# Performance work log

Measured on AMD Instinct MI355X. Metric: run time of the kernel, lower is better.

## Reference

```python
import jax, jax.numpy as jnp
import numpy as np

N = 4096
NODE_DIM = 256
HIDDEN = 64
N_CLASSES = 16
N_HEADS = 4
NEG_SLOPE = 0.01  # F.leaky_relu default


def _xavier(key, shape):
    fan_out, fan_in = shape[0], shape[1]
    limit = float(np.sqrt(6.0 / (fan_in + fan_out)))
    return jax.random.uniform(key, shape, jnp.float32, -limit, limit)


def setup_inputs() -> dict:
    key = jax.random.key(0)
    ks = jax.random.split(key, 8)
    x = jax.random.normal(ks[0], (N, NODE_DIM), jnp.float32)
    adj_mat = jax.random.randint(ks[1], (N, N), 0, 2, jnp.int32)
    # head-stacked layer-1 params
    W1 = _xavier(ks[2], (N_HEADS * HIDDEN, NODE_DIM)).reshape(N_HEADS, HIDDEN, NODE_DIM)
    a1_1 = _xavier(ks[3], (N_HEADS * HIDDEN, 1)).reshape(N_HEADS, HIDDEN)
    a2_1 = _xavier(ks[4], (N_HEADS * HIDDEN, 1)).reshape(N_HEADS, HIDDEN)
    # layer-2 params
    W2 = _xavier(ks[5], (N_CLASSES, N_HEADS * HIDDEN))
    a1_2 = _xavier(ks[6], (N_CLASSES, 1))[:, 0]
    a2_2 = _xavier(ks[7], (N_CLASSES, 1))[:, 0]
    return {"x": x, "adj_mat": adj_mat, "W1": W1, "a1_1": a1_1, "a2_1": a2_1,
            "W2": W2, "a1_2": a1_2, "a2_2": a2_2}


def _attention_layer(x, adj_f, W, a1, a2):
    # x: [N, in_dim], W: [out_dim, in_dim], a1/a2: [out_dim]
    h = x @ W.T                               # [N, d]
    f1 = h @ a1                               # [N]
    f2 = h @ a2                               # [N]
    e = jax.nn.leaky_relu(f1[:, None] + f2[None, :], NEG_SLOPE)  # [N, N]
    e = e * adj_f
    e = jnp.where(e == 0, -jnp.inf, e)        # faithful to torch.where(e==0, -inf, e)
    alpha = jax.nn.softmax(e, axis=1)         # [N, N]
    return alpha @ h                          # [N, d]


def reference(x, adj_mat, W1, a1_1, a2_1, W2, a1_2, a2_2):
    adj_f = adj_mat.astype(x.dtype)
    # layer 1: vmap over heads, concat along feature dim
    heads = jax.vmap(_attention_layer, in_axes=(None, None, 0, 0, 0))(
        x, adj_f, W1, a1_1, a2_1)              # [H, N, hidden]
    h = jnp.transpose(heads, (1, 0, 2)).reshape(N, N_HEADS * HIDDEN)
    h = jax.nn.elu(h)
    # dropout p=0.0 -> identity
    logits = _attention_layer(h, adj_f, W2, a1_2, a2_2)  # [N, n_classes]
    return logits
```

## Files before the change

kernel.cpp:

```cpp
#include <hip/hip_runtime.h>
#include <cstdint>

typedef __bf16 bf16x8 __attribute__((ext_vector_type(8)));
typedef float  f32x4  __attribute__((ext_vector_type(4)));

#define LOG2E 1.4426950408889634f

__device__ __forceinline__ void split8(const float* v, bf16x8& hi, bf16x8& lo) {
    union { bf16x8 v; __bf16 e[8]; } h, l;
    #pragma unroll
    for (int j = 0; j < 8; j++) {
        __bf16 hb = (__bf16)v[j];
        float  r  = v[j] - (float)hb;
        h.e[j] = hb; l.e[j] = (__bf16)r;
    }
    hi = h.v; lo = l.v;
}
__device__ __forceinline__ bf16x8 cvt8(const float* v) {
    union { bf16x8 v; __bf16 e[8]; } u;
    #pragma unroll
    for (int j = 0; j < 8; j++) u.e[j] = (__bf16)v[j];
    return u.v;
}
__device__ __forceinline__ void splitstore(unsigned short* ph, unsigned short* pl, float v) {
    __bf16 hb = (__bf16)v;
    float  r  = v - (float)hb;
    __bf16 lb = (__bf16)r;
    unsigned short hu, lu;
    __builtin_memcpy(&hu, &hb, 2); __builtin_memcpy(&lu, &lb, 2);
    *ph = hu; *pl = lu;
}
__device__ __forceinline__ unsigned short f2bfh(float v) {
    __bf16 hb = (__bf16)v; unsigned short hu;
    __builtin_memcpy(&hu, &hb, 2); return hu;
}

__global__ __launch_bounds__(256)
void kzero(float4* __restrict__ p) {
    p[blockIdx.x * 256 + threadIdx.x] = float4{0.f, 0.f, 0.f, 0.f};
}

__global__ __launch_bounds__(256)
void kpre(const int* __restrict__ adj, unsigned long long* __restrict__ bm64,
          const float* __restrict__ w1, const float* __restrict__ w2,
          unsigned short* __restrict__ w1h, unsigned short* __restrict__ w1l,
          unsigned short* __restrict__ w2h, unsigned short* __restrict__ w2l) {
    int bx = blockIdx.x, tid = threadIdx.x;
    if (bx < 8192) {
        int row = bx >> 1, jbase = (bx & 1) * 2048;
        int wave = tid >> 6, lane = tid & 63;
        const int* base = adj + (size_t)row * 4096 + jbase + wave * 512;
        unsigned long long* bmw = bm64 + row * 64 + (jbase >> 6) + wave * 8;
        #pragma unroll
        for (int it = 0; it < 8; it++) {
            int v = base[it * 64 + lane];
            unsigned long long mask = __ballot(v != 0);
            if (lane == 0) bmw[it] = mask;
        }
        return;
    }
    int e = ((bx - 8192) * 256 + tid) * 4;
    const float* src; unsigned short *dh, *dl;
    if (e < 65536) { src = w1 + e; dh = w1h + e; dl = w1l + e; }
    else { int e2 = e - 65536; src = w2 + e2; dh = w2h + e2; dl = w2l + e2; }
    #pragma unroll
    for (int j = 0; j < 4; j++) splitstore(dh + j, dl + j, src[j]);
}

__global__ __launch_bounds__(256)
void k1_gemm(const float* __restrict__ x,
             const unsigned short* __restrict__ w1h,
             const unsigned short* __restrict__ w1l,
             const float* __restrict__ a11, const float* __restrict__ a21,
             unsigned short* __restrict__ h1t_hi, float* __restrict__ fvals) {
    int tid = threadIdx.x, wave = tid >> 6, lane = tid & 63;
    int q = lane >> 4, m = lane & 15;
    int i0 = blockIdx.x * 16;
    int c0 = wave * 64;
    f32x4 acc[4] = {};
    #pragma unroll
    for (int k0 = 0; k0 < 256; k0 += 32) {
        bf16x8 ah, al;
        split8(x + (i0 + m) * 256 + k0 + q * 8, ah, al);
        #pragma unroll
        for (int ct = 0; ct < 4; ct++) {
            bf16x8 bh = *(const bf16x8*)(w1h + (c0 + ct * 16 + m) * 256 + k0 + q * 8);
            bf16x8 bl = *(const bf16x8*)(w1l + (c0 + ct * 16 + m) * 256 + k0 + q * 8);
            acc[ct] = __builtin_amdgcn_mfma_f32_16x16x32_bf16(ah, bh, acc[ct], 0, 0, 0);
            acc[ct] = __builtin_amdgcn_mfma_f32_16x16x32_bf16(al, bh, acc[ct], 0, 0, 0);
            acc[ct] = __builtin_amdgcn_mfma_f32_16x16x32_bf16(ah, bl, acc[ct], 0, 0, 0);
        }
    }
    float a1v[4], a2v[4];
    #pragma unroll
    for (int ct = 0; ct < 4; ct++) {
        a1v[ct] = a11[wave * 64 + ct * 16 + m];
        a2v[ct] = a21[wave * 64 + ct * 16 + m];
    }
    #pragma unroll
    for (int r = 0; r < 4; r++) {
        int i = i0 + q * 4 + r;
        float s1 = 0.f, s2 = 0.f;
        #pragma unroll
        for (int ct = 0; ct < 4; ct++) {
            int c = c0 + ct * 16 + m;
            h1t_hi[c * 4096 + i] = f2bfh(acc[ct][r]);
            s1 += acc[ct][r] * a1v[ct];
            s2 += acc[ct][r] * a2v[ct];
        }
        #pragma unroll
        for (int off = 1; off < 16; off <<= 1) {
            s1 += __shfl_xor(s1, off);
            s2 += __shfl_xor(s2, off);
        }
        if (m == 0) {
            fvals[wave * 4096 + i] = s1 * LOG2E;
            fvals[16384 + wave * 4096 + i] = s2 * LOG2E;
        }
    }
}

template<int NCT, int JLEN, bool ATOM>
__global__ __launch_bounds__(256)
void attn_kernel(const unsigned char* __restrict__ bmb,
                 const float* __restrict__ f1_all,
                 const float* __restrict__ f2_all,
                 const unsigned short* __restrict__ BTh_all,
                 float* __restrict__ pacc,
                 float* __restrict__ zacc,
                 int pstride) {
    constexpr int S    = JLEN / 32;
    constexpr int ST   = (S % 8 == 0) ? S + 4 : S;
    constexpr int PR   = S / 4;
    constexpr int R    = 64;
    constexpr int NU4  = R * PR;
    constexpr int CR   = NCT * 16;
    constexpr int TSTR = 40;
    constexpr int NIT  = JLEN / 32;
    int tid = threadIdx.x, wave = tid >> 6, lane = tid & 63;
    int q = lane >> 4, m = lane & 15;
    int head = blockIdx.y;
    int i0 = blockIdx.x * R;
    int jstart = blockIdx.z * JLEN;

    if (!ATOM) {
        pacc += (size_t)blockIdx.z * (size_t)(4096 * pstride);
        zacc += (size_t)blockIdx.z * (size_t)((NCT == 4 ? 4 : 1) * 4096);
    }

    __shared__ unsigned int ldsbm[R * ST];
    __shared__ unsigned short ldsbt[2][CR * TSTR];
    __shared__ float ldsf2[JLEN];

    const unsigned short* BTh = BTh_all + (size_t)head * CR * 4096;
    const float* f1 = f1_all + head * 4096;
    const float* f2 = f2_all + head * 4096;

    for (int c = tid; c < NU4; c += 256) {
        int row = c / PR, part = c % PR;
        uint4 v = *(const uint4*)(bmb + (size_t)(i0 + row) * 512 + (jstart >> 3) + part * 16);
        *(uint4*)&ldsbm[row * ST + part * 4] = v;
    }
    for (int c = tid; c < JLEN / 4; c += 256)
        *(float4*)&ldsf2[c * 4] = *(const float4*)(f2 + jstart + c * 4);

    int sc = tid >> 2, sp = tid & 3;
    bool stager = tid < CR * 4;
    const unsigned short* sbase = BTh + (size_t)sc * 4096 + jstart + sp * 8;
    unsigned short* swr = &ldsbt[0][0] + sc * TSTR + sp * 8;

    uint4 vA, vB;
    if (stager) {
        uint4 v0 = *(const uint4*)(sbase);
        *(uint4*)(swr) = v0;
        if (NIT > 1) vB = *(const uint4*)(sbase + 32);
    }

    int col0 = head * CR;
    int r0 = wave * 16;
    float f1s0 = f1[i0 + r0 + m];

    f32x4 acc0[NCT] = {};
    float z0 = 0.f;

    constexpr int BUFO = CR * TSTR;

    auto body = [&](int it, uint4& vpre, uint4& vwr) {
        __syncthreads();
        int jl = it * 32;
        if (stager && it + 2 < NIT)
            vpre = *(const uint4*)(sbase + jl + 64);
        unsigned int md0 = ldsbm[(r0 + m) * ST + it];
        const float4* f2p = (const float4*)&ldsf2[jl + q * 8];
        float4 fa = f2p[0], fb = f2p[1];
        float fv[8] = {fa.x, fa.y, fa.z, fa.w, fb.x, fb.y, fb.z, fb.w};
        float pv0[8];
        #pragma unroll
        for (int jj = 0; jj < 8; jj++) {
            int bit = q * 8 + jj;
            float s0 = f1s0 + fv[jj];
            float e0 = fmaxf(s0, 0.01f * s0);
            bool v0 = ((md0 >> bit) & 1u) && (s0 != 0.0f);
            float p0 = v0 ? __builtin_amdgcn_exp2f(e0) : 0.0f;
            z0 += p0; pv0[jj] = p0;
        }
        bf16x8 ah0 = cvt8(pv0);
        int cur = it & 1;
        const unsigned short* rb = &ldsbt[0][0] + cur * BUFO;
        #pragma unroll
        for (int ct = 0; ct < NCT; ct++) {
            bf16x8 bh = *(const bf16x8*)(rb + (ct * 16 + m) * TSTR + q * 8);
            acc0[ct] = __builtin_amdgcn_mfma_f32_16x16x32_bf16(ah0, bh, acc0[ct], 0, 0, 0);
        }
        if (stager && it + 1 < NIT)
            *(uint4*)(swr + (1 - cur) * BUFO) = vwr;
    };

    for (int itp = 0; itp < NIT; itp += 2) {
        body(itp,     vA, vB);
        body(itp + 1, vB, vA);
    }

    z0 += __shfl_xor(z0, 16); z0 += __shfl_xor(z0, 32);
    if (lane < 16) {
        if (ATOM) {
            atomicAdd(&zacc[head * 4096 + i0 + r0 + lane], z0);
        } else {
            zacc[head * 4096 + i0 + r0 + lane] = z0;
        }
    }
    #pragma unroll
    for (int ct = 0; ct < NCT; ct++)
        #pragma unroll
        for (int r = 0; r < 4; r++) {
            int col = col0 + ct * 16 + m;
            int rowA = i0 + r0 + q * 4 + r;
            if (ATOM) {
                atomicAdd(&pacc[rowA * pstride + col], acc0[ct][r]);
            } else {
                pacc[rowA * pstride + col] = acc0[ct][r];
            }
        }
}

__global__ __launch_bounds__(256)
void fin1c(const float* __restrict__ pp, const float* __restrict__ zp, int nj,
           unsigned short* __restrict__ hh, unsigned short* __restrict__ hl) {
    int row = blockIdx.x, col = threadIdx.x;
    float s = 0.f;
    for (int jc = 0; jc < nj; jc++) s += pp[(size_t)jc * (4096 * 256) + row * 256 + col];
    int head = col >> 6;
    float zz = 0.f;
    for (int jc = 0; jc < nj; jc++) zz += zp[jc * (4 * 4096) + head * 4096 + row];
    float v = s / zz;
    v = (v > 0.f) ? v : (__expf(v) - 1.0f);
    splitstore(&hh[row * 256 + col], &hl[row * 256 + col], v);
}

__global__ __launch_bounds__(256)
void k3_layer2(const unsigned short* __restrict__ helu_hi,
               const unsigned short* __restrict__ helu_lo,
               const unsigned short* __restrict__ w2h,
               const unsigned short* __restrict__ w2l,
               const float* __restrict__ a12,
               const float* __restrict__ a22,
               unsigned short* __restrict__ h2t_hi,
               float* __restrict__ fq) {
    int tid = threadIdx.x, wave = tid >> 6, lane = tid & 63;
    int q = lane >> 4, m = lane & 15;
    int i0 = (blockIdx.x * 4 + wave) * 16;
    f32x4 acc = {};
    #pragma unroll
    for (int k0 = 0; k0 < 256; k0 += 32) {
        bf16x8 ah = *(const bf16x8*)(helu_hi + (i0 + m) * 256 + k0 + q * 8);
        bf16x8 al = *(const bf16x8*)(helu_lo + (i0 + m) * 256 + k0 + q * 8);
        bf16x8 bh = *(const bf16x8*)(w2h + m * 256 + k0 + q * 8);
        bf16x8 bl = *(const bf16x8*)(w2l + m * 256 + k0 + q * 8);
        acc = __builtin_amdgcn_mfma_f32_16x16x32_bf16(ah, bh, acc, 0, 0, 0);
        acc = __builtin_amdgcn_mfma_f32_16x16x32_bf16(al, bh, acc, 0, 0, 0);
        acc = __builtin_amdgcn_mfma_f32_16x16x32_bf16(ah, bl, acc, 0, 0, 0);
    }
    float a1v = a12[m], a2v = a22[m];
    #pragma unroll
    for (int r = 0; r < 4; r++) {
        float v = acc[r];
        int i = i0 + q * 4 + r;
        h2t_hi[m * 4096 + i] = f2bfh(v);
        float s1 = v * a1v, s2 = v * a2v;
        #pragma unroll
        for (int off = 1; off < 16; off <<= 1) {
            s1 += __shfl_xor(s1, off);
            s2 += __shfl_xor(s2, off);
        }
        if (m == 0) { fq[i] = s1 * LOG2E; fq[4096 + i] = s2 * LOG2E; }
    }
}

__global__ __launch_bounds__(256)
void fin2(const float* __restrict__ pp, const float* __restrict__ zp, int nj,
          float* __restrict__ out) {
    int idx = blockIdx.x * 256 + threadIdx.x;
    float s = 0.f;
    for (int jc = 0; jc < nj; jc++) s += pp[jc * 65536 + idx];
    float zz = 0.f;
    for (int jc = 0; jc < nj; jc++) zz += zp[jc * 4096 + (idx >> 4)];
    out[idx] = s / zz;
}

extern "C" void kernel_launch(void* const* d_in, const int* in_sizes, int n_in,
                              void* d_out, int out_size, void* d_ws, size_t ws_size,
                              hipStream_t stream) {
    const float* x   = (const float*)d_in[0];
    const int*   adj = (const int*)d_in[1];
    const float* w1  = (const float*)d_in[2];
    const float* a11 = (const float*)d_in[3];
    const float* a21 = (const float*)d_in[4];
    const float* w2  = (const float*)d_in[5];
    const float* a12 = (const float*)d_in[6];
    const float* a22 = (const float*)d_in[7];
    float* out = (float*)d_out;

    uint8_t* w = (uint8_t*)d_ws;
    unsigned long long* bm  = (unsigned long long*)(w);
    unsigned short* h1t_hi  = (unsigned short*)(w + (2u << 20));
    unsigned short* h2t_hi  = (unsigned short*)(w + (4u << 20));
    float*          fvals   = (float*)(w + (4u << 20) + (128u << 10));
    float*          fq      = (float*)(w + (4u << 20) + (256u << 10));
    unsigned short* w1h     = (unsigned short*)(w + (4u << 20) + (288u << 10));
    unsigned short* w1l     = (unsigned short*)(w + (4u << 20) + (416u << 10));
    unsigned short* w2h     = (unsigned short*)(w + (4u << 20) + (544u << 10));
    unsigned short* w2l     = (unsigned short*)(w + (4u << 20) + (552u << 10));
    unsigned short* helu_hi = (unsigned short*)(w + (4u << 20) + (560u << 10));
    unsigned short* helu_lo = (unsigned short*)(w + (4u << 20) + (2608u << 10));

    bool big = ws_size >= ((size_t)48 << 20);
    float* p1 = (float*)(w + (9u << 20));
    float *z1, *p2, *z2;
    if (big) {
        z1 = p1 + (size_t)4 * 4096 * 256;
        p2 = z1 + 4 * 4 * 4096;
        z2 = p2 + (size_t)16 * 4096 * 16;
    } else {
        z1 = p1 + 4096 * 256;
        p2 = z1 + 4 * 4096;
        z2 = p2 + 4096 * 16;
    }

    if (!big) kzero<<<1108, 256, 0, stream>>>((float4*)p1);
    kpre<<<8260, 256, 0, stream>>>(adj, bm, w1, w2, w1h, w1l, w2h, w2l);
    k1_gemm<<<256, 256, 0, stream>>>(x, w1h, w1l, a11, a21, h1t_hi, fvals);
    if (big)
        attn_kernel<4, 1024, false><<<dim3(64, 4, 4), 256, 0, stream>>>(
            (const unsigned char*)bm, fvals, fvals + 16384, h1t_hi, p1, z1, 256);
    else
        attn_kernel<4, 1024, true><<<dim3(64, 4, 4), 256, 0, stream>>>(
            (const unsigned char*)bm, fvals, fvals + 16384, h1t_hi, p1, z1, 256);
    fin1c<<<4096, 256, 0, stream>>>(p1, z1, big ? 4 : 1, helu_hi, helu_lo);
    k3_layer2<<<64, 256, 0, stream>>>(helu_hi, helu_lo, w2h, w2l, a12, a22,
                                      h2t_hi, fq);
    if (big)
        attn_kernel<1, 256, false><<<dim3(64, 1, 16), 256, 0, stream>>>(
            (const unsigned char*)bm, fq, fq + 4096, h2t_hi, p2, z2, 16);
    else
        attn_kernel<1, 256, true><<<dim3(64, 1, 16), 256, 0, stream>>>(
            (const unsigned char*)bm, fq, fq + 4096, h2t_hi, p2, z2, 16);
    fin2<<<256, 256, 0, stream>>>(p2, z2, big ? 16 : 1, out);
}
```

Measured before the change: 190.9 us.

## Fuse layer-1 GEMM into adjacency prep and widen attention K-step to 64

Merges the weight-splitting preprocessing and the layer-1 GEMM into the adjacency bitmask kernel. The GEMM blocks now split W1 to hi/lo bf16 inline, and layer 2 splits W2 inline too, which removes a launch and the workspace round-trip for the split weights. The attention kernel now stages 64-column tiles per iteration with two 32-column MFMA sub-steps, and replaces __syncthreads with explicit lgkmcnt waits plus raw s_barrier, halving the number of barriers. The trade-off is redundant W1 conversion work in every GEMM block and larger LDS tiles, and the hand-placed waits risk subtle synchronization errors.

```diff
diff --git a/kernel.cpp b/kernel.cpp
--- a/kernel.cpp
+++ b/kernel.cpp
@@ -5,6 +5,8 @@
 typedef float  f32x4  __attribute__((ext_vector_type(4)));
 
 #define LOG2E 1.4426950408889634f
+#define LGKM0 do { asm volatile("s_waitcnt lgkmcnt(0)" ::: "memory"); \
+                   __builtin_amdgcn_sched_barrier(0); } while (0)
 
 __device__ __forceinline__ void split8(const float* v, bf16x8& hi, bf16x8& lo) {
     union { bf16x8 v; __bf16 e[8]; } h, l;
@@ -41,82 +43,69 @@
 }
 
 __global__ __launch_bounds__(256)
-void kpre(const int* __restrict__ adj, unsigned long long* __restrict__ bm64,
-          const float* __restrict__ w1, const float* __restrict__ w2,
-          unsigned short* __restrict__ w1h, unsigned short* __restrict__ w1l,
-          unsigned short* __restrict__ w2h, unsigned short* __restrict__ w2l) {
+void kpre2(const int* __restrict__ adj, unsigned long long* __restrict__ bm64,
+           const float* __restrict__ x, const float* __restrict__ w1,
+           const float* __restrict__ a11, const float* __restrict__ a21,
+           unsigned short* __restrict__ h1t_hi, float* __restrict__ fvals) {
     int bx = blockIdx.x, tid = threadIdx.x;
-    if (bx < 8192) {
-        int row = bx >> 1, jbase = (bx & 1) * 2048;
+    if (bx < 256) {
         int wave = tid >> 6, lane = tid & 63;
-        const int* base = adj + (size_t)row * 4096 + jbase + wave * 512;
-        unsigned long long* bmw = bm64 + row * 64 + (jbase >> 6) + wave * 8;
-        #pragma unroll
-        for (int it = 0; it < 8; it++) {
-            int v = base[it * 64 + lane];
-            unsigned long long mask = __ballot(v != 0);
-            if (lane == 0) bmw[it] = mask;
+        int q = lane >> 4, m = lane & 15;
+        int i0 = bx * 16;
+        int c0 = wave * 64;
+        f32x4 acc[4] = {};
+        #pragma unroll
+        for (int k0 = 0; k0 < 256; k0 += 32) {
+            bf16x8 ah, al;
+            split8(x + (i0 + m) * 256 + k0 + q * 8, ah, al);
+            #pragma unroll
+            for (int ct = 0; ct < 4; ct++) {
+                bf16x8 bh, bl;
+                split8(w1 + (c0 + ct * 16 + m) * 256 + k0 + q * 8, bh, bl);
+                acc[ct] = __builtin_amdgcn_mfma_f32_16x16x32_bf16(ah, bh, acc[ct], 0, 0, 0);
+                acc[ct] = __builtin_amdgcn_mfma_f32_16x16x32_bf16(al, bh, acc[ct], 0, 0, 0);
+                acc[ct] = __builtin_amdgcn_mfma_f32_16x16x32_bf16(ah, bl, acc[ct], 0, 0, 0);
+            }
+        }
+        float a1v[4], a2v[4];
+        #pragma unroll
+        for (int ct = 0; ct < 4; ct++) {
+            a1v[ct] = a11[wave * 64 + ct * 16 + m];
+            a2v[ct] = a21[wave * 64 + ct * 16 + m];
+        }
+        #pragma unroll
+        for (int r = 0; r < 4; r++) {
+            int i = i0 + q * 4 + r;
+            float s1 = 0.f, s2 = 0.f;
+            #pragma unroll
+            for (int ct = 0; ct < 4; ct++) {
+                int c = c0 + ct * 16 + m;
+                h1t_hi[c * 4096 + i] = f2bfh(acc[ct][r]);
+                s1 += acc[ct][r] * a1v[ct];
+                s2 += acc[ct][r] * a2v[ct];
+            }
+            #pragma unroll
+            for (int off = 1; off < 16; off <<= 1) {
+                s1 += __shfl_xor(s1, off);
+                s2 += __shfl_xor(s2, off);
+            }
+            if (m == 0) {
+                fvals[wave * 4096 + i] = s1 * LOG2E;
+                fvals[16384 + wave * 4096 + i] = s2 * LOG2E;
+            }
         }
         return;
     }
-    int e = ((bx - 8192) * 256 + tid) * 4;
-    const float* src; unsigned short *dh, *dl;
-    if (e < 65536) { src = w1 + e; dh = w1h + e; dl = w1l + e; }
-    else { int e2 = e - 65536; src = w2 + e2; dh = w2h + e2; dl = w2l + e2; }
-    #pragma unroll
-    for (int j = 0; j < 4; j++) splitstore(dh + j, dl + j, src[j]);
-}
-
-__global__ __launch_bounds__(256)
-void k1_gemm(const float* __restrict__ x,
-             const unsigned short* __restrict__ w1h,
-             const unsigned short* __restrict__ w1l,
-             const float* __restrict__ a11, const float* __restrict__ a21,
-             unsigned short* __restrict__ h1t_hi, float* __restrict__ fvals) {
-    int tid = threadIdx.x, wave = tid >> 6, lane = tid & 63;
-    int q = lane >> 4, m = lane & 15;
-    int i0 = blockIdx.x * 16;
-    int c0 = wave * 64;
-    f32x4 acc[4] = {};
-    #pragma unroll
-    for (int k0 = 0; k0 < 256; k0 += 32) {
-        bf16x8 ah, al;
-        split8(x + (i0 + m) * 256 + k0 + q * 8, ah, al);
-        #pragma unroll
-        for (int ct = 0; ct < 4; ct++) {
-            bf16x8 bh = *(const bf16x8*)(w1h + (c0 + ct * 16 + m) * 256 + k0 + q * 8);
-            bf16x8 bl = *(const bf16x8*)(w1l + (c0 + ct * 16 + m) * 256 + k0 + q * 8);
-            acc[ct] = __builtin_amdgcn_mfma_f32_16x16x32_bf16(ah, bh, acc[ct], 0, 0, 0);
-            acc[ct] = __builtin_amdgcn_mfma_f32_16x16x32_bf16(al, bh, acc[ct], 0, 0, 0);
-            acc[ct] = __builtin_amdgcn_mfma_f32_16x16x32_bf16(ah, bl, acc[ct], 0, 0, 0);
-        }
-    }
-    float a1v[4], a2v[4];
-    #pragma unroll
-    for (int ct = 0; ct < 4; ct++) {
-        a1v[ct] = a11[wave * 64 + ct * 16 + m];
-        a2v[ct] = a21[wave * 64 + ct * 16 + m];
-    }
-    #pragma unroll
-    for (int r = 0; r < 4; r++) {
-        int i = i0 + q * 4 + r;
-        float s1 = 0.f, s2 = 0.f;
-        #pragma unroll
-        for (int ct = 0; ct < 4; ct++) {
-            int c = c0 + ct * 16 + m;
-            h1t_hi[c * 4096 + i] = f2bfh(acc[ct][r]);
-            s1 += acc[ct][r] * a1v[ct];
-            s2 += acc[ct][r] * a2v[ct];
-        }
-        #pragma unroll
-        for (int off = 1; off < 16; off <<= 1) {
-            s1 += __shfl_xor(s1, off);
-            s2 += __shfl_xor(s2, off);
-        }
-        if (m == 0) {
-            fvals[wave * 4096 + i] = s1 * LOG2E;
-            fvals[16384 + wave * 4096 + i] = s2 * LOG2E;
-        }
+    int bxa = bx - 256;
+    int row = bxa >> 1, jbase = (bxa & 1) * 2048;
+    int wave = tid >> 6, lane = tid & 63;
+    const int* base = adj + (size_t)row * 4096 + jbase + wave * 512;
+    unsigned long long* bmw = bm64 + row * 64 + (jbase >> 6) + wave * 8;
+    #pragma unroll
+    for (int it = 0; it < 8; it++) {
+        int v = base[it * 64 + lane];
+        unsigned long long mask = __ballot(v != 0);
+        if (lane == 0) bmw[it] = mask;
     }
 }
 
@@ -135,8 +124,9 @@
     constexpr int R    = 64;
     constexpr int NU4  = R * PR;
     constexpr int CR   = NCT * 16;
-    constexpr int TSTR = 40;
-    constexpr int NIT  = JLEN / 32;
+    constexpr int TSTR = 72;
+    constexpr int NIT  = JLEN / 64;
+    constexpr int BUFO = CR * TSTR;
     int tid = threadIdx.x, wave = tid >> 6, lane = tid & 63;
     int q = lane >> 4, m = lane & 15;
     int head = blockIdx.y;
@@ -149,7 +139,7 @@
     }
 
     __shared__ unsigned int ldsbm[R * ST];
-    __shared__ unsigned short ldsbt[2][CR * TSTR];
+    __shared__ unsigned short ldsbt[2][BUFO];
     __shared__ float ldsf2[JLEN];
 
     const unsigned short* BTh = BTh_all + (size_t)head * CR * 4096;
@@ -165,15 +155,18 @@
         *(float4*)&ldsf2[c * 4] = *(const float4*)(f2 + jstart + c * 4);
 
     int sc = tid >> 2, sp = tid & 3;
-    bool stager = tid < CR * 4;
+    bool stager = (NCT == 4) ? true : (tid < CR * 4);
     const unsigned short* sbase = BTh + (size_t)sc * 4096 + jstart + sp * 8;
-    unsigned short* swr = &ldsbt[0][0] + sc * TSTR + sp * 8;
-
-    uint4 vA, vB;
+    unsigned short* swr0 = &ldsbt[0][0] + sc * TSTR + sp * 8;
+
+    uint4 vA0, vA1, vB0, vB1;
     if (stager) {
-        uint4 v0 = *(const uint4*)(sbase);
-        *(uint4*)(swr) = v0;
-        if (NIT > 1) vB = *(const uint4*)(sbase + 32);
+        uint4 t00 = *(const uint4*)(sbase);
+        uint4 t01 = *(const uint4*)(sbase + 32);
+        *(uint4*)(swr0) = t00;
+        *(uint4*)(swr0 + 32) = t01;
+        vB0 = *(const uint4*)(sbase + 64);
+        vB1 = *(const uint4*)(sbase + 96);
     }
 
     int col0 = head * CR;
@@ -182,44 +175,71 @@
 
     f32x4 acc0[NCT] = {};
     float z0 = 0.f;
-
-    constexpr int BUFO = CR * TSTR;
-
-    auto body = [&](int it, uint4& vpre, uint4& vwr) {
-        __syncthreads();
-        int jl = it * 32;
-        if (stager && it + 2 < NIT)
-            vpre = *(const uint4*)(sbase + jl + 64);
-        unsigned int md0 = ldsbm[(r0 + m) * ST + it];
-        const float4* f2p = (const float4*)&ldsf2[jl + q * 8];
-        float4 fa = f2p[0], fb = f2p[1];
-        float fv[8] = {fa.x, fa.y, fa.z, fa.w, fb.x, fb.y, fb.z, fb.w};
-        float pv0[8];
-        #pragma unroll
-        for (int jj = 0; jj < 8; jj++) {
-            int bit = q * 8 + jj;
-            float s0 = f1s0 + fv[jj];
-            float e0 = fmaxf(s0, 0.01f * s0);
-            bool v0 = ((md0 >> bit) & 1u) && (s0 != 0.0f);
-            float p0 = v0 ? __builtin_amdgcn_exp2f(e0) : 0.0f;
-            z0 += p0; pv0[jj] = p0;
-        }
-        bf16x8 ah0 = cvt8(pv0);
-        int cur = it & 1;
+    int mrow = (r0 + m) * ST;
+
+    auto compute = [&](int it, int cur) {
+        int jl = it * 64;
+        unsigned long long mw = *(const unsigned long long*)&ldsbm[mrow + 2 * it];
         const unsigned short* rb = &ldsbt[0][0] + cur * BUFO;
         #pragma unroll
-        for (int ct = 0; ct < NCT; ct++) {
-            bf16x8 bh = *(const bf16x8*)(rb + (ct * 16 + m) * TSTR + q * 8);
-            acc0[ct] = __builtin_amdgcn_mfma_f32_16x16x32_bf16(ah0, bh, acc0[ct], 0, 0, 0);
-        }
-        if (stager && it + 1 < NIT)
-            *(uint4*)(swr + (1 - cur) * BUFO) = vwr;
+        for (int js = 0; js < 2; js++) {
+            unsigned int md0 = (js == 0) ? (unsigned int)mw : (unsigned int)(mw >> 32);
+            const float4* f2p = (const float4*)&ldsf2[jl + js * 32 + q * 8];
+            float4 fa = f2p[0], fb = f2p[1];
+            float fv[8] = {fa.x, fa.y, fa.z, fa.w, fb.x, fb.y, fb.z, fb.w};
+            float pv0[8];
+            #pragma unroll
+            for (int jj = 0; jj < 8; jj++) {
+                int bit = q * 8 + jj;
+                float s0 = f1s0 + fv[jj];
+                float e0 = fmaxf(s0, 0.01f * s0);
+                bool v0 = ((md0 >> bit) & 1u) && (s0 != 0.0f);
+                float p0 = v0 ? __builtin_amdgcn_exp2f(e0) : 0.0f;
+                z0 += p0; pv0[jj] = p0;
+            }
+            bf16x8 ah0 = cvt8(pv0);
+            #pragma unroll
+            for (int ct = 0; ct < NCT; ct++) {
+                bf16x8 bh = *(const bf16x8*)(rb + (ct * 16 + m) * TSTR + js * 32 + q * 8);
+                acc0[ct] = __builtin_amdgcn_mfma_f32_16x16x32_bf16(ah0, bh, acc0[ct], 0, 0, 0);
+            }
+        }
     };
 
-    for (int itp = 0; itp < NIT; itp += 2) {
-        body(itp,     vA, vB);
-        body(itp + 1, vB, vA);
-    }
+    LGKM0;
+    for (int itp = 0; itp + 2 < NIT; itp += 2) {
+        __builtin_amdgcn_s_barrier();
+        if (stager) {
+            vA0 = *(const uint4*)(sbase + (itp + 2) * 64);
+            vA1 = *(const uint4*)(sbase + (itp + 2) * 64 + 32);
+        }
+        compute(itp, 0);
+        if (stager) {
+            *(uint4*)(swr0 + BUFO) = vB0;
+            *(uint4*)(swr0 + BUFO + 32) = vB1;
+        }
+        LGKM0;
+        __builtin_amdgcn_s_barrier();
+        if (stager) {
+            vB0 = *(const uint4*)(sbase + (itp + 3) * 64);
+            vB1 = *(const uint4*)(sbase + (itp + 3) * 64 + 32);
+        }
+        compute(itp + 1, 1);
+        if (stager) {
+            *(uint4*)(swr0) = vA0;
+            *(uint4*)(swr0 + 32) = vA1;
+        }
+        LGKM0;
+    }
+    __builtin_amdgcn_s_barrier();
+    compute(NIT - 2, 0);
+    if (stager) {
+        *(uint4*)(swr0 + BUFO) = vB0;
+        *(uint4*)(swr0 + BUFO + 32) = vB1;
+    }
+    LGKM0;
+    __builtin_amdgcn_s_barrier();
+    compute(NIT - 1, 1);
 
     z0 += __shfl_xor(z0, 16); z0 += __shfl_xor(z0, 32);
     if (lane < 16) {
@@ -260,8 +280,7 @@
 __global__ __launch_bounds__(256)
 void k3_layer2(const unsigned short* __restrict__ helu_hi,
                const unsigned short* __restrict__ helu_lo,
-               const unsigned short* __restrict__ w2h,
-               const unsigned short* __restrict__ w2l,
+               const float* __restrict__ w2,
                const float* __restrict__ a12,
                const float* __restrict__ a22,
                unsigned short* __restrict__ h2t_hi,
@@ -274,8 +293,8 @@
     for (int k0 = 0; k0 < 256; k0 += 32) {
         bf16x8 ah = *(const bf16x8*)(helu_hi + (i0 + m) * 256 + k0 + q * 8);
         bf16x8 al = *(const bf16x8*)(helu_lo + (i0 + m) * 256 + k0 + q * 8);
-        bf16x8 bh = *(const bf16x8*)(w2h + m * 256 + k0 + q * 8);
-        bf16x8 bl = *(const bf16x8*)(w2l + m * 256 + k0 + q * 8);
+        bf16x8 bh, bl;
+        split8(w2 + m * 256 + k0 + q * 8, bh, bl);
         acc = __builtin_amdgcn_mfma_f32_16x16x32_bf16(ah, bh, acc, 0, 0, 0);
         acc = __builtin_amdgcn_mfma_f32_16x16x32_bf16(al, bh, acc, 0, 0, 0);
         acc = __builtin_amdgcn_mfma_f32_16x16x32_bf16(ah, bl, acc, 0, 0, 0);
@@ -326,10 +345,6 @@
     unsigned short* h2t_hi  = (unsigned short*)(w + (4u << 20));
     float*          fvals   = (float*)(w + (4u << 20) + (128u << 10));
     float*          fq      = (float*)(w + (4u << 20) + (256u << 10));
-    unsigned short* w1h     = (unsigned short*)(w + (4u << 20) + (288u << 10));
-    unsigned short* w1l     = (unsigned short*)(w + (4u << 20) + (416u << 10));
-    unsigned short* w2h     = (unsigned short*)(w + (4u << 20) + (544u << 10));
-    unsigned short* w2l     = (unsigned short*)(w + (4u << 20) + (552u << 10));
     unsigned short* helu_hi = (unsigned short*)(w + (4u << 20) + (560u << 10));
     unsigned short* helu_lo = (unsigned short*)(w + (4u << 20) + (2608u << 10));
 
@@ -347,8 +362,7 @@
     }
 
     if (!big) kzero<<<1108, 256, 0, stream>>>((float4*)p1);
-    kpre<<<8260, 256, 0, stream>>>(adj, bm, w1, w2, w1h, w1l, w2h, w2l);
-    k1_gemm<<<256, 256, 0, stream>>>(x, w1h, w1l, a11, a21, h1t_hi, fvals);
+    kpre2<<<8448, 256, 0, stream>>>(adj, bm, x, w1, a11, a21, h1t_hi, fvals);
     if (big)
         attn_kernel<4, 1024, false><<<dim3(64, 4, 4), 256, 0, stream>>>(
             (const unsigned char*)bm, fvals, fvals + 16384, h1t_hi, p1, z1, 256);
@@ -356,7 +370,7 @@
         attn_kernel<4, 1024, true><<<dim3(64, 4, 4), 256, 0, stream>>>(
             (const unsigned char*)bm, fvals, fvals + 16384, h1t_hi, p1, z1, 256);
     fin1c<<<4096, 256, 0, stream>>>(p1, z1, big ? 4 : 1, helu_hi, helu_lo);
-    k3_layer2<<<64, 256, 0, stream>>>(helu_hi, helu_lo, w2h, w2l, a12, a22,
+    k3_layer2<<<64, 256, 0, stream>>>(helu_hi, helu_lo, w2, a12, a22,
                                       h2t_hi, fq);
     if (big)
         attn_kernel<1, 256, false><<<dim3(64, 1, 16), 256, 0, stream>>>(
```

New measurement: 182.9 us. 4.2% less time.
